# Kernel tuning notes

Measured on AMD Instinct MI355X. Metric: run time of the kernel, lower is better.

Reference implementation:

```python
import jax, jax.numpy as jnp
import numpy as np

D, N = 512, 65536


def setup_inputs() -> dict:
    key = jax.random.key(0)
    k1, k2 = jax.random.split(key)
    feats = jax.random.normal(k1, (D, N), dtype=jnp.float32)
    warped_feats = jax.random.normal(k2, (D, N), dtype=jnp.float32)
    return {"feats": feats, "warped_feats": warped_feats}


def reference(feats, warped_feats):
    # diag(feats.T @ warped_feats)[n] == sum_d feats[d,n] * warped_feats[d,n]
    # Same math as the torch module, without materializing the NxN matrix.
    diag = jnp.einsum('dn,dn->n', feats, warped_feats)  # [N]
    cosine = 1.0 - diag
    return cosine.mean()
```

## Files before the change

### kernel.cpp

```cpp
#include <hip/hip_runtime.h>

#define THREADS 512
#define BLOCKS  1024
#define ITERS   16
#define UNROLL  4

typedef float f32x4 __attribute__((ext_vector_type(4)));

__global__ __launch_bounds__(THREADS) void dot_partial_kernel(
        const f32x4* __restrict__ a,
        const f32x4* __restrict__ b,
        float* __restrict__ partial) {
    const int base = blockIdx.x * (ITERS * THREADS) + threadIdx.x;

    f32x4 acc0 = (f32x4)0.f, acc1 = (f32x4)0.f, acc2 = (f32x4)0.f, acc3 = (f32x4)0.f;

    #pragma unroll
    for (int i = 0; i < ITERS; i += UNROLL) {
        const int i0 = base + (i + 0) * THREADS;
        const int i1 = base + (i + 1) * THREADS;
        const int i2 = base + (i + 2) * THREADS;
        const int i3 = base + (i + 3) * THREADS;
        f32x4 a0 = __builtin_nontemporal_load(a + i0);
        f32x4 b0 = __builtin_nontemporal_load(b + i0);
        f32x4 a1 = __builtin_nontemporal_load(a + i1);
        f32x4 b1 = __builtin_nontemporal_load(b + i1);
        f32x4 a2 = __builtin_nontemporal_load(a + i2);
        f32x4 b2 = __builtin_nontemporal_load(b + i2);
        f32x4 a3 = __builtin_nontemporal_load(a + i3);
        f32x4 b3 = __builtin_nontemporal_load(b + i3);
        acc0 += a0 * b0;
        acc1 += a1 * b1;
        acc2 += a2 * b2;
        acc3 += a3 * b3;
    }

    f32x4 accv = (acc0 + acc1) + (acc2 + acc3);
    float s = (accv.x + accv.y) + (accv.z + accv.w);

    #pragma unroll
    for (int off = 32; off > 0; off >>= 1)
        s += __shfl_down(s, off, 64);

    __shared__ float smem[THREADS / 64];
    const int lane = threadIdx.x & 63;
    const int wave = threadIdx.x >> 6;
    if (lane == 0) smem[wave] = s;
    __syncthreads();

    if (threadIdx.x == 0) {
        float t = 0.f;
        #pragma unroll
        for (int w = 0; w < THREADS / 64; ++w) t += smem[w];
        partial[blockIdx.x] = t;
    }
}

__global__ __launch_bounds__(256) void final_reduce_kernel(
        const float* __restrict__ partial,
        float* __restrict__ out,
        int np, float inv_n) {
    float s = 0.f;
    for (int i = threadIdx.x; i < np; i += 256) s += partial[i];

    #pragma unroll
    for (int off = 32; off > 0; off >>= 1)
        s += __shfl_down(s, off, 64);

    __shared__ float smem[4];
    const int lane = threadIdx.x & 63;
    const int wave = threadIdx.x >> 6;
    if (lane == 0) smem[wave] = s;
    __syncthreads();

    if (threadIdx.x == 0) {
        float t = 0.f;
        #pragma unroll
        for (int w = 0; w < 4; ++w) t += smem[w];
        out[0] = 1.0f - t * inv_n;
    }
}

extern "C" void kernel_launch(void* const* d_in, const int* in_sizes, int n_in,
                              void* d_out, int out_size, void* d_ws, size_t ws_size,
                              hipStream_t stream) {
    const float* feats  = (const float*)d_in[0];
    const float* warped = (const float*)d_in[1];
    float* out = (float*)d_out;
    float* ws  = (float*)d_ws;

    const float inv_n = 1.0f / 65536.0f;

    dot_partial_kernel<<<BLOCKS, THREADS, 0, stream>>>(
        (const f32x4*)feats, (const f32x4*)warped, ws);
    final_reduce_kernel<<<1, 256, 0, stream>>>(ws, out, BLOCKS, inv_n);
}
```

Before: 248.9 us.

## Fuse final reduction into partial kernel using last-block ticket counter

Removes the second kernel launch by having each block atomically bump a global ticket after writing its partial sum. The last block to arrive reads all 1024 partials and writes the final mean. This saves one launch and its gap, at the cost of one atomic per block and a small serial tail in the last block. The ticket is reset so the kernel can be called again.

New measurement: 294.7 us. 1.18x slower.

```diff
diff --git a/kernel.cpp b/kernel.cpp
--- a/kernel.cpp
+++ b/kernel.cpp
@@ -7,10 +7,14 @@
 
 typedef float f32x4 __attribute__((ext_vector_type(4)));
 
-__global__ __launch_bounds__(THREADS) void dot_partial_kernel(
+__device__ unsigned int g_ticket = 0;
+
+__global__ __launch_bounds__(THREADS) void dot_fused_kernel(
         const f32x4* __restrict__ a,
         const f32x4* __restrict__ b,
-        float* __restrict__ partial) {
+        float* __restrict__ partial,
+        float* __restrict__ out,
+        float inv_n) {
     const int base = blockIdx.x * (ITERS * THREADS) + threadIdx.x;
 
     f32x4 acc0 = (f32x4)0.f, acc1 = (f32x4)0.f, acc2 = (f32x4)0.f, acc3 = (f32x4)0.f;
@@ -43,6 +47,7 @@
         s += __shfl_down(s, off, 64);
 
     __shared__ float smem[THREADS / 64];
+    __shared__ unsigned int ticket;
     const int lane = threadIdx.x & 63;
     const int wave = threadIdx.x >> 6;
     if (lane == 0) smem[wave] = s;
@@ -52,32 +57,34 @@
         float t = 0.f;
         #pragma unroll
         for (int w = 0; w < THREADS / 64; ++w) t += smem[w];
-        partial[blockIdx.x] = t;
+        __hip_atomic_store(&partial[blockIdx.x], t, __ATOMIC_RELAXED,
+                           __HIP_MEMORY_SCOPE_AGENT);
+        ticket = __hip_atomic_fetch_add(&g_ticket, 1u, __ATOMIC_ACQ_REL,
+                                        __HIP_MEMORY_SCOPE_AGENT);
     }
-}
-
-__global__ __launch_bounds__(256) void final_reduce_kernel(
-        const float* __restrict__ partial,
-        float* __restrict__ out,
-        int np, float inv_n) {
-    float s = 0.f;
-    for (int i = threadIdx.x; i < np; i += 256) s += partial[i];
-
-    #pragma unroll
-    for (int off = 32; off > 0; off >>= 1)
-        s += __shfl_down(s, off, 64);
-
-    __shared__ float smem[4];
-    const int lane = threadIdx.x & 63;
-    const int wave = threadIdx.x >> 6;
-    if (lane == 0) smem[wave] = s;
     __syncthreads();
 
-    if (threadIdx.x == 0) {
-        float t = 0.f;
+    if (ticket == BLOCKS - 1) {
+        float r = __hip_atomic_load(&partial[threadIdx.x], __ATOMIC_RELAXED,
+                                    __HIP_MEMORY_SCOPE_AGENT)
+                + __hip_atomic_load(&partial[threadIdx.x + THREADS], __ATOMIC_RELAXED,
+                                    __HIP_MEMORY_SCOPE_AGENT);
+
         #pragma unroll
-        for (int w = 0; w < 4; ++w) t += smem[w];
-        out[0] = 1.0f - t * inv_n;
+        for (int off = 32; off > 0; off >>= 1)
+            r += __shfl_down(r, off, 64);
+
+        if (lane == 0) smem[wave] = r;
+        __syncthreads();
+
+        if (threadIdx.x == 0) {
+            float t = 0.f;
+            #pragma unroll
+            for (int w = 0; w < THREADS / 64; ++w) t += smem[w];
+            out[0] = 1.0f - t * inv_n;
+            __hip_atomic_store(&g_ticket, 0u, __ATOMIC_RELAXED,
+                               __HIP_MEMORY_SCOPE_AGENT);
+        }
     }
 }
 
@@ -91,7 +98,6 @@
 
     const float inv_n = 1.0f / 65536.0f;
 
-    dot_partial_kernel<<<BLOCKS, THREADS, 0, stream>>>(
-        (const f32x4*)feats, (const f32x4*)warped, ws);
-    final_reduce_kernel<<<1, 256, 0, stream>>>(ws, out, BLOCKS, inv_n);
+    dot_fused_kernel<<<BLOCKS, THREADS, 0, stream>>>(
+        (const f32x4*)feats, (const f32x4*)warped, ws, out, inv_n);
 }
```
